# Kernel optimization log

Measured on AMD Instinct MI355X. Metric: run time of the kernel, lower is better.

The kernel has to match this reference:

```python
import jax, jax.numpy as jnp
import numpy as np

D_MODEL = 2048
N_HEADS = 16
D_HEAD = D_MODEL // N_HEADS
D_FF = 4 * D_MODEL
LN_EPS = 1e-5


def setup_inputs() -> dict:
    key = jax.random.key(0)
    ks = jax.random.split(key, 12)
    s = 1.0 / np.sqrt(D_MODEL)
    sf = 1.0 / np.sqrt(D_FF)
    return {
        "x": jax.random.normal(ks[0], (1, 2048, D_MODEL), dtype=jnp.float32),
        "ln1_g": jnp.ones((D_MODEL,), jnp.float32),
        "ln1_b": jnp.zeros((D_MODEL,), jnp.float32),
        # weights stored [in, out] (transpose of torch layout; equivalent under random init)
        "Wq": jax.random.normal(ks[1], (D_MODEL, D_MODEL), jnp.float32) * s,
        "Wk": jax.random.normal(ks[2], (D_MODEL, D_MODEL), jnp.float32) * s,
        "Wv": jax.random.normal(ks[3], (D_MODEL, D_MODEL), jnp.float32) * s,
        "Wp": jax.random.normal(ks[4], (D_MODEL, D_MODEL), jnp.float32) * s,
        "bp": jnp.zeros((D_MODEL,), jnp.float32),
        "ln2_g": jnp.ones((D_MODEL,), jnp.float32),
        "ln2_b": jnp.zeros((D_MODEL,), jnp.float32),
        "W1": jax.random.normal(ks[5], (D_MODEL, D_FF), jnp.float32) * s,
        "b1": jnp.zeros((D_FF,), jnp.float32),
        "W2": jax.random.normal(ks[6], (D_FF, D_MODEL), jnp.float32) * sf,
        "b2": jnp.zeros((D_MODEL,), jnp.float32),
    }


def _layer_norm(x, g, b):
    mu = jnp.mean(x, axis=-1, keepdims=True)
    var = jnp.mean(jnp.square(x - mu), axis=-1, keepdims=True)
    return (x - mu) * jax.lax.rsqrt(var + LN_EPS) * g + b


def _attention(h, Wq, Wk, Wv, Wp, bp):
    B, S, E = h.shape
    q = (h @ Wq).reshape(B, S, N_HEADS, D_HEAD)
    k = (h @ Wk).reshape(B, S, N_HEADS, D_HEAD)
    v = (h @ Wv).reshape(B, S, N_HEADS, D_HEAD)
    # [B, H, S, S] causal scores (matches the naive materialized original)
    scores = jnp.einsum("bqhd,bkhd->bhqk", q, k) / np.sqrt(D_HEAD).astype(np.float32)
    causal = jnp.arange(S)[:, None] >= jnp.arange(S)[None, :]
    scores = jnp.where(causal, scores, -jnp.inf)
    attn = jax.nn.softmax(scores, axis=-1)
    out = jnp.einsum("bhqk,bkhd->bqhd", attn, v).reshape(B, S, E)
    return out @ Wp + bp


def reference(x, ln1_g, ln1_b, Wq, Wk, Wv, Wp, bp, ln2_g, ln2_b, W1, b1, W2, b2):
    # attention branch: x += MHA(LN1(x)); dropout=0 (inference)
    x1 = x + _attention(_layer_norm(x, ln1_g, ln1_b), Wq, Wk, Wv, Wp, bp)
    # ff branch: FeedForward adds its own residual on the normalized input
    g = _layer_norm(x1, ln2_g, ln2_b)
    mlp = jax.nn.gelu(g @ W1 + b1, approximate=False) @ W2 + b2
    return x1 + (g + mlp)
```

## Files before the change

### kernel.cpp

```cpp
#include <hip/hip_runtime.h>
#include <math.h>

typedef unsigned int u32;
typedef unsigned short u16;
typedef __attribute__((ext_vector_type(8))) short short8;
typedef __attribute__((ext_vector_type(4))) float f32x4;

__device__ __forceinline__ u16 f2bf(float f) {
  u32 u = __builtin_bit_cast(u32, f);
  u += 0x7FFFu + ((u >> 16) & 1u);
  return (u16)(u >> 16);
}
__device__ __forceinline__ float bf2f(u16 h) {
  u32 u = ((u32)h) << 16;
  return __builtin_bit_cast(float, u);
}
__device__ __forceinline__ void gload_lds16(const void* g, void* l) {
  __builtin_amdgcn_global_load_lds((const __attribute__((address_space(1))) u32*)g,
                                   (__attribute__((address_space(3))) u32*)l, 16, 0, 0);
}
__device__ __forceinline__ f32x4 mfma16(short8 a, short8 b, f32x4 c) {
  return __builtin_amdgcn_mfma_f32_16x16x32_bf16(a, b, c, 0, 0, 0);
}

__global__ __launch_bounds__(256) void transpose_cast4(const float* __restrict__ Wq,
                                                       const float* __restrict__ Wk,
                                                       const float* __restrict__ Wv,
                                                       const float* __restrict__ Wp,
                                                       u16* __restrict__ wqkvT,
                                                       u16* __restrict__ wpT) {
  __shared__ __attribute__((aligned(16))) u16 tile[64][72];
  const int z = blockIdx.z;
  const float* src = (z == 0) ? Wq : (z == 1) ? Wk : (z == 2) ? Wv : Wp;
  u16* dst = (z < 3) ? (wqkvT + (size_t)z * 2048 * 2048) : wpT;
  const int n0 = blockIdx.x * 64, k0 = blockIdx.y * 64;
  const int t = threadIdx.x;
  const int tr = t >> 4;
  const int tc4 = (t & 15) * 4;
#pragma unroll
  for (int p = 0; p < 4; ++p) {
    int row = p * 16 + tr;
    const float4 v = *(const float4*)(src + (size_t)(k0 + row) * 2048 + n0 + tc4);
    tile[tc4 + 0][row] = f2bf(v.x);
    tile[tc4 + 1][row] = f2bf(v.y);
    tile[tc4 + 2][row] = f2bf(v.z);
    tile[tc4 + 3][row] = f2bf(v.w);
  }
  __syncthreads();
  const int nr = t >> 2;
  const int kc = (t & 3) * 16;
  u16* d = dst + (size_t)(n0 + nr) * 2048 + k0 + kc;
  *(short8*)(d) = *(const short8*)&tile[nr][kc];
  *(short8*)(d + 8) = *(const short8*)&tile[nr][kc + 8];
}

__global__ __launch_bounds__(256) void transpose_cast(const float* __restrict__ src,
                                                      u16* __restrict__ dst, int K, int N) {
  __shared__ __attribute__((aligned(16))) u16 tile[64][72];
  const int n0 = blockIdx.x * 64, k0 = blockIdx.y * 64;
  const int t = threadIdx.x;
  const int tr = t >> 4;
  const int tc4 = (t & 15) * 4;
#pragma unroll
  for (int p = 0; p < 4; ++p) {
    int row = p * 16 + tr;
    const float4 v = *(const float4*)(src + (size_t)(k0 + row) * N + n0 + tc4);
    tile[tc4 + 0][row] = f2bf(v.x);
    tile[tc4 + 1][row] = f2bf(v.y);
    tile[tc4 + 2][row] = f2bf(v.z);
    tile[tc4 + 3][row] = f2bf(v.w);
  }
  __syncthreads();
  const int nr = t >> 2;
  const int kc = (t & 3) * 16;
  u16* d = dst + (size_t)(n0 + nr) * K + k0 + kc;
  *(short8*)(d) = *(const short8*)&tile[nr][kc];
  *(short8*)(d + 8) = *(const short8*)&tile[nr][kc + 8];
}

__global__ __launch_bounds__(256) void transpose_v(const u16* __restrict__ qkv,
                                                   u16* __restrict__ vT) {
  __shared__ __attribute__((aligned(16))) u16 tile[64][72];
  const int kv0 = blockIdx.x * 64, d0 = blockIdx.y * 64, h = blockIdx.z;
  const int t = threadIdx.x;
  const int tr = t >> 3;
  const int tc8 = (t & 7) * 8;
#pragma unroll
  for (int p = 0; p < 2; ++p) {
    int row = p * 32 + tr;
    short8 v = *(const short8*)(qkv + (size_t)(kv0 + row) * 6144 + 4096 + h * 128 + d0 + tc8);
#pragma unroll
    for (int j = 0; j < 8; ++j) tile[tc8 + j][row] = (u16)v[j];
  }
  __syncthreads();
  const int dr = t >> 2;
  const int kc = (t & 3) * 16;
  u16* dst = vT + ((size_t)h * 128 + d0 + dr) * 2048 + kv0 + kc;
  *(short8*)dst = *(const short8*)&tile[dr][kc];
  *(short8*)(dst + 8) = *(const short8*)&tile[dr][kc + 8];
}

__global__ __launch_bounds__(256) void ln_kernel(const float* __restrict__ x,
                                                 const float* __restrict__ gw,
                                                 const float* __restrict__ bw,
                                                 u16* __restrict__ out) {
  const int row = blockIdx.x, t = threadIdx.x;
  const float* xr = x + (size_t)row * 2048;
  const float4 v0 = *(const float4*)(xr + t * 8);
  const float4 v1 = *(const float4*)(xr + t * 8 + 4);
  float s = v0.x + v0.y + v0.z + v0.w + v1.x + v1.y + v1.z + v1.w;
  float q = v0.x * v0.x + v0.y * v0.y + v0.z * v0.z + v0.w * v0.w +
            v1.x * v1.x + v1.y * v1.y + v1.z * v1.z + v1.w * v1.w;
#pragma unroll
  for (int w = 32; w; w >>= 1) { s += __shfl_xor(s, w); q += __shfl_xor(q, w); }
  __shared__ float rs[4], rq[4];
  const int wid = t >> 6, lane = t & 63;
  if (!lane) { rs[wid] = s; rq[wid] = q; }
  __syncthreads();
  s = rs[0] + rs[1] + rs[2] + rs[3];
  q = rq[0] + rq[1] + rq[2] + rq[3];
  const float mu = s * (1.f / 2048.f);
  const float var = q * (1.f / 2048.f) - mu * mu;
  const float rstd = rsqrtf(var + 1e-5f);
  const float4 g0 = *(const float4*)(gw + t * 8);
  const float4 g1 = *(const float4*)(gw + t * 8 + 4);
  const float4 b0 = *(const float4*)(bw + t * 8);
  const float4 b1 = *(const float4*)(bw + t * 8 + 4);
  short8 o;
  o[0] = (short)f2bf((v0.x - mu) * rstd * g0.x + b0.x);
  o[1] = (short)f2bf((v0.y - mu) * rstd * g0.y + b0.y);
  o[2] = (short)f2bf((v0.z - mu) * rstd * g0.z + b0.z);
  o[3] = (short)f2bf((v0.w - mu) * rstd * g0.w + b0.w);
  o[4] = (short)f2bf((v1.x - mu) * rstd * g1.x + b1.x);
  o[5] = (short)f2bf((v1.y - mu) * rstd * g1.y + b1.y);
  o[6] = (short)f2bf((v1.z - mu) * rstd * g1.z + b1.z);
  o[7] = (short)f2bf((v1.w - mu) * rstd * g1.w + b1.w);
  *(short8*)(out + (size_t)row * 2048 + t * 8) = o;
}

__global__ __launch_bounds__(256) void reduce_ln(const float* __restrict__ pA,
                                                 const float* __restrict__ pB,
                                                 const float* __restrict__ bias,
                                                 const float* __restrict__ res1,
                                                 const float* __restrict__ gw,
                                                 const float* __restrict__ bw,
                                                 float* __restrict__ x1,
                                                 u16* __restrict__ g) {
  const int row = blockIdx.x, t = threadIdx.x;
  const size_t MN = 4194304;
  const size_t base = (size_t)row * 2048 + t * 8;
  float v[8];
#pragma unroll
  for (int half = 0; half < 2; ++half) {
    float4 a0 = *(const float4*)(pA + base + half * 4);
    float4 a1 = *(const float4*)(pA + MN + base + half * 4);
    float4 b0 = *(const float4*)(pB + base + half * 4);
    float4 b1 = *(const float4*)(pB + MN + base + half * 4);
    float4 bi = *(const float4*)(bias + t * 8 + half * 4);
    float4 r1 = *(const float4*)(res1 + base + half * 4);
    v[half * 4 + 0] = a0.x + a1.x + b0.x + b1.x + bi.x + r1.x;
    v[half * 4 + 1] = a0.y + a1.y + b0.y + b1.y + bi.y + r1.y;
    v[half * 4 + 2] = a0.z + a1.z + b0.z + b1.z + bi.z + r1.z;
    v[half * 4 + 3] = a0.w + a1.w + b0.w + b1.w + bi.w + r1.w;
  }
  float4 o0 = {v[0], v[1], v[2], v[3]}, o1 = {v[4], v[5], v[6], v[7]};
  *(float4*)(x1 + base) = o0;
  *(float4*)(x1 + base + 4) = o1;
  float s = 0.f, q = 0.f;
#pragma unroll
  for (int j = 0; j < 8; ++j) { s += v[j]; q += v[j] * v[j]; }
#pragma unroll
  for (int w = 32; w; w >>= 1) { s += __shfl_xor(s, w); q += __shfl_xor(q, w); }
  __shared__ float rs[4], rq[4];
  const int wid = t >> 6, lane = t & 63;
  if (!lane) { rs[wid] = s; rq[wid] = q; }
  __syncthreads();
  s = rs[0] + rs[1] + rs[2] + rs[3];
  q = rq[0] + rq[1] + rq[2] + rq[3];
  const float mu = s * (1.f / 2048.f);
  const float var = q * (1.f / 2048.f) - mu * mu;
  const float rstd = rsqrtf(var + 1e-5f);
  short8 o;
#pragma unroll
  for (int j = 0; j < 8; ++j) {
    float gj = *(gw + t * 8 + j);
    float bj = *(bw + t * 8 + j);
    o[j] = (short)f2bf((v[j] - mu) * rstd * gj + bj);
  }
  *(short8*)(g + base) = o;
}

template <int EPI>
__global__ __launch_bounds__(512, 2) void gemm3(const u16* __restrict__ A,
                                                const u16* __restrict__ Bt,
                                                int M, int N, int K, int Kc,
                                                u16* __restrict__ outB,
                                                const float* __restrict__ bias,
                                                float* __restrict__ pA,
                                                float* __restrict__ pB) {
  __shared__ __attribute__((aligned(16))) u16 lds[3 * 16384];
  const int m0 = blockIdx.y * 256, n0 = blockIdx.x * 256;
  const int tid = threadIdx.x, wid = tid >> 6, lane = tid & 63;
  const int wr = wid >> 2, wc = wid & 3;
  const int lq = lane & 15, lk = lane >> 4;
  const int kStart = blockIdx.z * Kc;
  const int NT = Kc / 32;

  size_t aoff[2], boff[2];
#pragma unroll
  for (int s = 0; s < 2; ++s) {
    int c = s * 512 + tid;
    int row = c >> 2;
    int col = ((c & 3) ^ ((row >> 1) & 3)) * 8;
    aoff[s] = (size_t)(m0 + row) * K + kStart + col;
    boff[s] = (size_t)(n0 + row) * K + kStart + col;
  }
  u16* ldst = lds + tid * 8;

#define STA(s, buf, t2) gload_lds16(A + aoff[s] + (size_t)((t2) * 32), \
                                    ldst + (buf) * 16384 + (s) * 4096)
#define STB(s, buf, t2) gload_lds16(Bt + boff[s] + (size_t)((t2) * 32), \
                                    ldst + (buf) * 16384 + 8192 + (s) * 4096)

  STA(0, 0, 0); STA(1, 0, 0); STB(0, 0, 0); STB(1, 0, 0);
  STA(0, 1, 1); STA(1, 1, 1); STB(0, 1, 1); STB(1, 1, 1);
  asm volatile("s_waitcnt vmcnt(4)" ::: "memory");
  __builtin_amdgcn_s_barrier();
  __builtin_amdgcn_sched_barrier(0);

  f32x4 acc[8][4] = {};
  int cur = 0, nxt2 = 2;
  for (int t = 0; t < NT; ++t) {
    const char* bufc = (const char*)lds + cur * 32768;
    const bool st = (t + 2) < NT;
    short8 bf[4], af[4];
#pragma unroll
    for (int ni = 0; ni < 4; ++ni) {
      int br = wc * 64 + ni * 16 + lq;
      bf[ni] = *(const short8*)(bufc + 16384 + br * 64 + ((lk ^ ((br >> 1) & 3)) << 4));
    }
#pragma unroll
    for (int mi = 0; mi < 4; ++mi) {
      int ar = wr * 128 + mi * 16 + lq;
      af[mi] = *(const short8*)(bufc + ar * 64 + ((lk ^ ((ar >> 1) & 3)) << 4));
    }
    if (st) { STA(0, nxt2, t + 2); STA(1, nxt2, t + 2); }
    __builtin_amdgcn_s_setprio(1);
#pragma unroll
    for (int mi = 0; mi < 4; ++mi)
#pragma unroll
      for (int ni = 0; ni < 4; ++ni)
        acc[mi][ni] = mfma16(af[mi], bf[ni], acc[mi][ni]);
    __builtin_amdgcn_s_setprio(0);
#pragma unroll
    for (int mi = 0; mi < 4; ++mi) {
      int ar = wr * 128 + (mi + 4) * 16 + lq;
      af[mi] = *(const short8*)(bufc + ar * 64 + ((lk ^ ((ar >> 1) & 3)) << 4));
    }
    if (st) { STB(0, nxt2, t + 2); STB(1, nxt2, t + 2); }
    __builtin_amdgcn_s_setprio(1);
#pragma unroll
    for (int mi = 0; mi < 4; ++mi)
#pragma unroll
      for (int ni = 0; ni < 4; ++ni)
        acc[mi + 4][ni] = mfma16(af[mi], bf[ni], acc[mi + 4][ni]);
    __builtin_amdgcn_s_setprio(0);
    if (st) asm volatile("s_waitcnt vmcnt(4)" ::: "memory");
    else    asm volatile("s_waitcnt vmcnt(0)" ::: "memory");
    __builtin_amdgcn_s_barrier();
    __builtin_amdgcn_sched_barrier(0);
    cur = (cur == 2) ? 0 : cur + 1;
    nxt2 = (nxt2 == 2) ? 0 : nxt2 + 1;
  }
#undef STA
#undef STB

  float* pp = nullptr;
  if (EPI == 4) {
    pp = (blockIdx.z < 2 ? pA : pB) + (size_t)(blockIdx.z & 1) * ((size_t)M * N);
  }
#pragma unroll
  for (int mi = 0; mi < 8; ++mi) {
#pragma unroll
    for (int ni = 0; ni < 4; ++ni) {
      const int col = n0 + wc * 64 + ni * 16 + lq;
#pragma unroll
      for (int r = 0; r < 4; ++r) {
        const int row = m0 + wr * 128 + mi * 16 + lk * 4 + r;
        const size_t idx = (size_t)row * N + col;
        float v = acc[mi][ni][r];
        if (EPI == 0) {
          outB[idx] = f2bf(v);
        } else if (EPI == 2) {
          float xg = v + bias[col];
          outB[idx] = f2bf(0.5f * xg * (1.f + erff(xg * 0.70710678118654752f)));
        } else {
          pp[idx] = v;
        }
      }
    }
  }
}

template <int NS, int RES2>
__global__ __launch_bounds__(256) void reduce_kernel(const float* __restrict__ pA,
                                                     const float* __restrict__ pB,
                                                     const float* __restrict__ bias,
                                                     const float* __restrict__ res1,
                                                     const u16* __restrict__ res2,
                                                     float* __restrict__ out,
                                                     int MN, int N) {
  const int i = (blockIdx.x * 256 + threadIdx.x) * 4;
  if (i >= MN) return;
  float4 s = *(const float4*)(pA + i);
  {
    const float4 t = *(const float4*)(pA + MN + i);
    s.x += t.x; s.y += t.y; s.z += t.z; s.w += t.w;
  }
  if (NS == 4) {
    const float4 t0 = *(const float4*)(pB + i);
    const float4 t1 = *(const float4*)(pB + MN + i);
    s.x += t0.x + t1.x; s.y += t0.y + t1.y; s.z += t0.z + t1.z; s.w += t0.w + t1.w;
  }
  const int col = i & (N - 1);
  const float4 bv = *(const float4*)(bias + col);
  const float4 r1 = *(const float4*)(res1 + i);
  float4 o;
  o.x = s.x + bv.x + r1.x;
  o.y = s.y + bv.y + r1.y;
  o.z = s.z + bv.z + r1.z;
  o.w = s.w + bv.w + r1.w;
  if (RES2) {
    const u16* r2 = res2 + i;
    o.x += bf2f(r2[0]); o.y += bf2f(r2[1]); o.z += bf2f(r2[2]); o.w += bf2f(r2[3]);
  }
  *(float4*)(out + i) = o;
}

__global__ __launch_bounds__(256) void attn_kernel(const u16* __restrict__ qkv,
                                                   const u16* __restrict__ vT,
                                                   u16* __restrict__ attnout) {
  __shared__ __attribute__((aligned(16))) u16 lsK[2 * 64 * 128];
  __shared__ __attribute__((aligned(16))) u16 lsV[2 * 128 * 64];
  __shared__ __attribute__((aligned(16))) u16 lsP[4][16 * 64];
  const int h = blockIdx.x;
  const int qi = 31 - blockIdx.y;
  const int qb = qi * 64;
  const int tid = threadIdx.x, wid = tid >> 6, lane = tid & 63;
  const int lq = lane & 15, lk = lane >> 4;
  const int qw = qb + wid * 16;

  short8 qf[4];
  {
    const u16* qp = qkv + (size_t)(qw + lq) * 6144 + h * 128;
#pragma unroll
    for (int ks = 0; ks < 4; ++ks) qf[ks] = *(const short8*)(qp + ks * 32 + lk * 8);
  }
  float mreg[4], lreg[4];
  f32x4 o[8];
#pragma unroll
  for (int r = 0; r < 4; ++r) { mreg[r] = -INFINITY; lreg[r] = 0.f; }
#pragma unroll
  for (int dt = 0; dt < 8; ++dt) o[dt] = (f32x4){0.f, 0.f, 0.f, 0.f};

  const int rK = lane >> 4, sK = lane & 15;
  const int rV = lane >> 3, sV = lane & 7;
  const int nkt = qi + 1;

  auto STAGE = [&](int kt_, int b_) {
    const int kv0_ = kt_ * 64;
#pragma unroll
    for (int i = 0; i < 4; ++i) {
      int c = wid * 4 + i;
      int rowK = c * 4 + rK;
      gload_lds16(qkv + (size_t)(kv0_ + rowK) * 6144 + 2048 + h * 128 + ((sK ^ (rowK & 7)) * 8),
                  lsK + b_ * 8192 + c * 512);
      int rowV = c * 8 + rV;
      gload_lds16(vT + ((size_t)h * 128 + rowV) * 2048 + kv0_ + ((sV ^ (rowV & 7)) * 8),
                  lsV + b_ * 8192 + c * 512);
    }
  };

  STAGE(0, 0);
  for (int kt = 0; kt < nkt; ++kt) {
    const int b = kt & 1;
    const int kv0 = kt * 64;
    if (kt + 1 < nkt) {
      STAGE(kt + 1, b ^ 1);
      asm volatile("s_waitcnt vmcnt(8)" ::: "memory");
    } else {
      asm volatile("s_waitcnt vmcnt(0)" ::: "memory");
    }
    __builtin_amdgcn_s_barrier();
    __builtin_amdgcn_sched_barrier(0);
    const char* Kb = (const char*)(lsK + b * 8192);
    const char* Vb = (const char*)(lsV + b * 8192);

    f32x4 sc[4];
#pragma unroll
    for (int nt = 0; nt < 4; ++nt) sc[nt] = (f32x4){0.f, 0.f, 0.f, 0.f};
#pragma unroll
    for (int ks = 0; ks < 4; ++ks) {
#pragma unroll
      for (int nt = 0; nt < 4; ++nt) {
        int kvr = nt * 16 + lq;
        short8 kf = *(const short8*)(Kb + kvr * 256 +
                                     ((ks * 64 + lk * 16) ^ ((kvr & 7) << 4)));
        sc[nt] = mfma16(qf[ks], kf, sc[nt]);
      }
    }
    float rmax[4] = {-INFINITY, -INFINITY, -INFINITY, -INFINITY};
#pragma unroll
    for (int nt = 0; nt < 4; ++nt) {
      int kv = kv0 + nt * 16 + lq;
#pragma unroll
      for (int r = 0; r < 4; ++r) {
        int qrow = qw + lk * 4 + r;
        float s = (kv <= qrow) ? sc[nt][r] * 0.08838834764831845f : -INFINITY;
        sc[nt][r] = s;
        rmax[r] = fmaxf(rmax[r], s);
      }
    }
#pragma unroll
    for (int r = 0; r < 4; ++r)
#pragma unroll
      for (int w = 1; w < 16; w <<= 1) rmax[r] = fmaxf(rmax[r], __shfl_xor(rmax[r], w));
    bool grow = false;
#pragma unroll
    for (int r = 0; r < 4; ++r) grow |= (rmax[r] > mreg[r] + 8.f);
    if (__any(grow)) {
#pragma unroll
      for (int r = 0; r < 4; ++r) {
        float mn = fmaxf(mreg[r], rmax[r]);
        float alpha = __expf(mreg[r] - mn);
        mreg[r] = mn;
        lreg[r] *= alpha;
#pragma unroll
        for (int dt = 0; dt < 8; ++dt) o[dt][r] *= alpha;
      }
    }
    float rsum[4] = {0.f, 0.f, 0.f, 0.f};
    u16* P = &lsP[wid][0];
#pragma unroll
    for (int nt = 0; nt < 4; ++nt) {
#pragma unroll
      for (int r = 0; r < 4; ++r) {
        float p = __expf(sc[nt][r] - mreg[r]);
        rsum[r] += p;
        int prow = lk * 4 + r, pcol = nt * 16 + lq;
        *(u16*)((char*)P + prow * 128 + ((pcol * 2) ^ ((prow & 7) << 4))) = f2bf(p);
      }
    }
#pragma unroll
    for (int r = 0; r < 4; ++r) {
#pragma unroll
      for (int w = 1; w < 16; w <<= 1) rsum[r] += __shfl_xor(rsum[r], w);
      lreg[r] += rsum[r];
    }
#pragma unroll
    for (int kk = 0; kk < 2; ++kk) {
      short8 pa = *(const short8*)((const char*)P + lq * 128 +
                                   ((kk * 64 + lk * 16) ^ ((lq & 7) << 4)));
#pragma unroll
      for (int dt = 0; dt < 8; ++dt) {
        int dr = dt * 16 + lq;
        short8 vf = *(const short8*)(Vb + dr * 128 +
                                     ((kk * 64 + lk * 16) ^ ((dr & 7) << 4)));
        o[dt] = mfma16(pa, vf, o[dt]);
      }
    }
    __builtin_amdgcn_s_barrier();
  }
#pragma unroll
  for (int r = 0; r < 4; ++r) {
    float inv = 1.f / lreg[r];
    int row = qw + lk * 4 + r;
    u16* op = attnout + (size_t)row * 2048 + h * 128 + lq;
#pragma unroll
    for (int dt = 0; dt < 8; ++dt) op[dt * 16] = f2bf(o[dt][r] * inv);
  }
}

extern "C" void kernel_launch(void* const* d_in, const int* in_sizes, int n_in,
                              void* d_out, int out_size, void* d_ws, size_t ws_size,
                              hipStream_t stream) {
  (void)in_sizes; (void)n_in; (void)out_size; (void)ws_size;
  const float* x    = (const float*)d_in[0];
  const float* ln1g = (const float*)d_in[1];
  const float* ln1b = (const float*)d_in[2];
  const float* Wq   = (const float*)d_in[3];
  const float* Wk   = (const float*)d_in[4];
  const float* Wv   = (const float*)d_in[5];
  const float* Wp   = (const float*)d_in[6];
  const float* bp   = (const float*)d_in[7];
  const float* ln2g = (const float*)d_in[8];
  const float* ln2b = (const float*)d_in[9];
  const float* W1   = (const float*)d_in[10];
  const float* b1   = (const float*)d_in[11];
  const float* W2   = (const float*)d_in[12];
  const float* b2   = (const float*)d_in[13];
  float* out = (float*)d_out;
  char* ws = (char*)d_ws;

  u16* wqkvT = (u16*)(ws + 0);
  u16* hbuf  = (u16*)(ws + 25165824);
  u16* wpT   = (u16*)(ws + 33554432);
  u16* w1T   = (u16*)(ws + 41943040);
  u16* w2T   = (u16*)(ws + 75497472);
  u16* qkv   = (u16*)(ws + 109051904);
  u16* vT    = (u16*)(ws + 134217728);
  u16* attn  = (u16*)(ws + 142606336);
  float* x1  = (float*)(ws + 150994944);
  u16* g     = (u16*)(ws + 167772160);
  u16* ff1   = (u16*)(ws + 0);
  float* projPA = (float*)(ws + 0);
  float* projPB = (float*)(ws + 109051904);
  float* ffPA = (float*)(ws + 33554432);
  float* ffPB = (float*)(ws + 109051904);

  dim3 b256(256), b512(512);
  transpose_cast4<<<dim3(32, 32, 4), b256, 0, stream>>>(Wq, Wk, Wv, Wp, wqkvT, wpT);
  transpose_cast<<<dim3(128, 32), b256, 0, stream>>>(W1, w1T, 2048, 8192);
  transpose_cast<<<dim3(32, 128), b256, 0, stream>>>(W2, w2T, 8192, 2048);
  ln_kernel<<<2048, b256, 0, stream>>>(x, ln1g, ln1b, hbuf);
  gemm3<0><<<dim3(24, 8, 1), b512, 0, stream>>>(hbuf, wqkvT, 2048, 6144, 2048, 2048,
                                                qkv, nullptr, nullptr, nullptr);
  transpose_v<<<dim3(32, 2, 16), b256, 0, stream>>>(qkv, vT);
  attn_kernel<<<dim3(16, 32), b256, 0, stream>>>(qkv, vT, attn);
  gemm3<4><<<dim3(8, 8, 4), b512, 0, stream>>>(attn, wpT, 2048, 2048, 2048, 512,
                                               nullptr, nullptr, projPA, projPB);
  reduce_ln<<<2048, b256, 0, stream>>>(projPA, projPB, bp, x, ln2g, ln2b, x1, g);
  gemm3<2><<<dim3(32, 8, 1), b512, 0, stream>>>(g, w1T, 2048, 8192, 2048, 2048,
                                                ff1, b1, nullptr, nullptr);
  gemm3<4><<<dim3(8, 8, 4), b512, 0, stream>>>(ff1, w2T, 2048, 2048, 8192, 2048,
                                               nullptr, nullptr, ffPA, ffPB);
  reduce_kernel<4, 1><<<4096, b256, 0, stream>>>(ffPA, ffPB, b2, x1, g, out,
                                                 4194304, 2048);
}
```

Baseline: 413.2 us.

## Split attention KV range across two blocks with merge kernel; add smaller-tile QKV GEMM

Attention now splits each query tile's causal KV range into two chunks processed by separate blocks. Each block writes unnormalized fp32 partial outputs plus row max and sum, and a new merge kernel combines the two halves into bf16. The aim is more parallelism and better load balance for the causal workload. In exchange it drops the double-buffered K/V prefetch, and the extra fp32 partial traffic plus an added launch cost memory bandwidth. Separately, the QKV projection switches to a new gemm5 with 256x128 tiles and a 3-stage LDS pipeline, doubling the grid to raise occupancy.

```diff
diff --git a/kernel.cpp b/kernel.cpp
--- a/kernel.cpp
+++ b/kernel.cpp
@@ -302,6 +302,109 @@
   }
 }
 
+template <int EPI>
+__global__ __launch_bounds__(512, 4) void gemm5(const u16* __restrict__ A,
+                                                const u16* __restrict__ Bt,
+                                                int M, int N, int K, int Kc,
+                                                u16* __restrict__ outB,
+                                                const float* __restrict__ bias,
+                                                float* __restrict__ pA,
+                                                float* __restrict__ pB) {
+  __shared__ __attribute__((aligned(16))) u16 lds[3 * 12288];
+  const int m0 = blockIdx.y * 256, n0 = blockIdx.x * 128;
+  const int tid = threadIdx.x, wid = tid >> 6, lane = tid & 63;
+  const int wr = wid >> 1, wc = wid & 1;
+  const int lq = lane & 15, lk = lane >> 4;
+  const int kStart = blockIdx.z * Kc;
+  const int NT = Kc / 32;
+
+  size_t aoff[2], boff;
+#pragma unroll
+  for (int s = 0; s < 2; ++s) {
+    int c = s * 512 + tid;
+    int row = c >> 2;
+    int col = ((c & 3) ^ ((row >> 1) & 3)) * 8;
+    aoff[s] = (size_t)(m0 + row) * K + kStart + col;
+  }
+  {
+    int row = tid >> 2;
+    int col = ((tid & 3) ^ ((row >> 1) & 3)) * 8;
+    boff = (size_t)(n0 + row) * K + kStart + col;
+  }
+  u16* ldst = lds + tid * 8;
+
+#define STA(s, buf, t2) gload_lds16(A + aoff[s] + (size_t)((t2) * 32), \
+                                    ldst + (buf) * 12288 + (s) * 4096)
+#define STB(buf, t2) gload_lds16(Bt + boff + (size_t)((t2) * 32), \
+                                 ldst + (buf) * 12288 + 8192)
+
+  STA(0, 0, 0); STA(1, 0, 0); STB(0, 0);
+  STA(0, 1, 1); STA(1, 1, 1); STB(1, 1);
+  asm volatile("s_waitcnt vmcnt(3)" ::: "memory");
+  __builtin_amdgcn_s_barrier();
+  __builtin_amdgcn_sched_barrier(0);
+
+  f32x4 acc[4][4] = {};
+  int cur = 0, nxt2 = 2;
+  for (int t = 0; t < NT; ++t) {
+    const char* bufc = (const char*)lds + cur * 24576;
+    const bool st = (t + 2) < NT;
+    short8 bf[4], af[4];
+#pragma unroll
+    for (int ni = 0; ni < 4; ++ni) {
+      int br = wc * 64 + ni * 16 + lq;
+      bf[ni] = *(const short8*)(bufc + 16384 + br * 64 + ((lk ^ ((br >> 1) & 3)) << 4));
+    }
+#pragma unroll
+    for (int mi = 0; mi < 4; ++mi) {
+      int ar = wr * 64 + mi * 16 + lq;
+      af[mi] = *(const short8*)(bufc + ar * 64 + ((lk ^ ((ar >> 1) & 3)) << 4));
+    }
+    if (st) { STA(0, nxt2, t + 2); STA(1, nxt2, t + 2); STB(nxt2, t + 2); }
+    __builtin_amdgcn_s_setprio(1);
+#pragma unroll
+    for (int mi = 0; mi < 4; ++mi)
+#pragma unroll
+      for (int ni = 0; ni < 4; ++ni)
+        acc[mi][ni] = mfma16(af[mi], bf[ni], acc[mi][ni]);
+    __builtin_amdgcn_s_setprio(0);
+    if (st) asm volatile("s_waitcnt vmcnt(3)" ::: "memory");
+    else    asm volatile("s_waitcnt vmcnt(0)" ::: "memory");
+    __builtin_amdgcn_s_barrier();
+    __builtin_amdgcn_sched_barrier(0);
+    cur = (cur == 2) ? 0 : cur + 1;
+    nxt2 = (nxt2 == 2) ? 0 : nxt2 + 1;
+  }
+#undef STA
+#undef STB
+
+  float* pp = nullptr;
+  if (EPI == 4) {
+    pp = (blockIdx.z < 2 ? pA : pB) + (size_t)(blockIdx.z & 1) * ((size_t)M * N);
+  }
+#pragma unroll
+  for (int mi = 0; mi < 4; ++mi) {
+#pragma unroll
+    for (int ni = 0; ni < 4; ++ni) {
+      const int col = n0 + wc * 64 + ni * 16 + lq;
+#pragma unroll
+      for (int r = 0; r < 4; ++r) {
+        const int row = m0 + wr * 64 + mi * 16 + lk * 4 + r;
+        const size_t idx = (size_t)row * N + col;
+        float v = acc[mi][ni][r];
+        if (EPI == 0) {
+          outB[idx] = f2bf(v);
+        } else if (EPI == 2) {
+          float xg = v + bias[col];
+          outB[idx] = f2bf(0.5f * xg * (1.f + erff(xg * 0.70710678118654752f)));
+        } else {
+          pp[idx] = v;
+        }
+      }
+    }
+  }
+}
+
 template <int NS, int RES2>
 __global__ __launch_bounds__(256) void reduce_kernel(const float* __restrict__ pA,
                                                      const float* __restrict__ pB,
@@ -339,17 +442,25 @@
 
 __global__ __launch_bounds__(256) void attn_kernel(const u16* __restrict__ qkv,
                                                    const u16* __restrict__ vT,
-                                                   u16* __restrict__ attnout) {
-  __shared__ __attribute__((aligned(16))) u16 lsK[2 * 64 * 128];
-  __shared__ __attribute__((aligned(16))) u16 lsV[2 * 128 * 64];
+                                                   float* __restrict__ po,
+                                                   float* __restrict__ pm,
+                                                   float* __restrict__ pl) {
+  __shared__ __attribute__((aligned(16))) u16 lsK[64 * 128];
+  __shared__ __attribute__((aligned(16))) u16 lsV[128 * 64];
   __shared__ __attribute__((aligned(16))) u16 lsP[4][16 * 64];
   const int h = blockIdx.x;
-  const int qi = 31 - blockIdx.y;
+  const int c = blockIdx.y;
+  const int qi = 31 - blockIdx.z;
   const int qb = qi * 64;
   const int tid = threadIdx.x, wid = tid >> 6, lane = tid & 63;
   const int lq = lane & 15, lk = lane >> 4;
   const int qw = qb + wid * 16;
 
+  const int nkt = qi + 1;
+  const int ch0 = (nkt + 1) >> 1;
+  const int base = c ? ch0 : 0;
+  const int cnt = c ? (nkt - ch0) : ch0;
+
   short8 qf[4];
   {
     const u16* qp = qkv + (size_t)(qw + lq) * 6144 + h * 128;
@@ -365,36 +476,21 @@
 
   const int rK = lane >> 4, sK = lane & 15;
   const int rV = lane >> 3, sV = lane & 7;
-  const int nkt = qi + 1;
-
-  auto STAGE = [&](int kt_, int b_) {
-    const int kv0_ = kt_ * 64;
+  for (int it = 0; it < cnt; ++it) {
+    const int kt = base + it;
+    const int kv0 = kt * 64;
+    if (it) __syncthreads();
 #pragma unroll
     for (int i = 0; i < 4; ++i) {
-      int c = wid * 4 + i;
-      int rowK = c * 4 + rK;
-      gload_lds16(qkv + (size_t)(kv0_ + rowK) * 6144 + 2048 + h * 128 + ((sK ^ (rowK & 7)) * 8),
-                  lsK + b_ * 8192 + c * 512);
-      int rowV = c * 8 + rV;
-      gload_lds16(vT + ((size_t)h * 128 + rowV) * 2048 + kv0_ + ((sV ^ (rowV & 7)) * 8),
-                  lsV + b_ * 8192 + c * 512);
-    }
-  };
-
-  STAGE(0, 0);
-  for (int kt = 0; kt < nkt; ++kt) {
-    const int b = kt & 1;
-    const int kv0 = kt * 64;
-    if (kt + 1 < nkt) {
-      STAGE(kt + 1, b ^ 1);
-      asm volatile("s_waitcnt vmcnt(8)" ::: "memory");
-    } else {
-      asm volatile("s_waitcnt vmcnt(0)" ::: "memory");
-    }
-    __builtin_amdgcn_s_barrier();
-    __builtin_amdgcn_sched_barrier(0);
-    const char* Kb = (const char*)(lsK + b * 8192);
-    const char* Vb = (const char*)(lsV + b * 8192);
+      int cc = wid * 4 + i;
+      int rowK = cc * 4 + rK;
+      gload_lds16(qkv + (size_t)(kv0 + rowK) * 6144 + 2048 + h * 128 + ((sK ^ (rowK & 7)) * 8),
+                  lsK + cc * 512);
+      int rowV = cc * 8 + rV;
+      gload_lds16(vT + ((size_t)h * 128 + rowV) * 2048 + kv0 + ((sV ^ (rowV & 7)) * 8),
+                  lsV + cc * 512);
+    }
+    __syncthreads();
 
     f32x4 sc[4];
 #pragma unroll
@@ -404,7 +500,7 @@
 #pragma unroll
       for (int nt = 0; nt < 4; ++nt) {
         int kvr = nt * 16 + lq;
-        short8 kf = *(const short8*)(Kb + kvr * 256 +
+        short8 kf = *(const short8*)((const char*)lsK + kvr * 256 +
                                      ((ks * 64 + lk * 16) ^ ((kvr & 7) << 4)));
         sc[nt] = mfma16(qf[ks], kf, sc[nt]);
       }
@@ -464,21 +560,45 @@
 #pragma unroll
       for (int dt = 0; dt < 8; ++dt) {
         int dr = dt * 16 + lq;
-        short8 vf = *(const short8*)(Vb + dr * 128 +
+        short8 vf = *(const short8*)((const char*)lsV + dr * 128 +
                                      ((kk * 64 + lk * 16) ^ ((dr & 7) << 4)));
         o[dt] = mfma16(pa, vf, o[dt]);
       }
     }
-    __builtin_amdgcn_s_barrier();
   }
 #pragma unroll
   for (int r = 0; r < 4; ++r) {
-    float inv = 1.f / lreg[r];
     int row = qw + lk * 4 + r;
-    u16* op = attnout + (size_t)row * 2048 + h * 128 + lq;
-#pragma unroll
-    for (int dt = 0; dt < 8; ++dt) op[dt * 16] = f2bf(o[dt][r] * inv);
-  }
+    float* op = po + (size_t)c * 4194304 + ((size_t)h * 2048 + row) * 128 + lq;
+#pragma unroll
+    for (int dt = 0; dt < 8; ++dt) op[dt * 16] = o[dt][r];
+    if (lq == 0) {
+      pm[c * 32768 + h * 2048 + row] = mreg[r];
+      pl[c * 32768 + h * 2048 + row] = lreg[r];
+    }
+  }
+}
+
+__global__ __launch_bounds__(256) void attn_merge(const float* __restrict__ po,
+                                                  const float* __restrict__ pm,
+                                                  const float* __restrict__ pl,
+                                                  u16* __restrict__ attn) {
+  const int e = (blockIdx.x * 256 + threadIdx.x) * 4;
+  const int hrow = e >> 7;
+  const int d = e & 127;
+  const int h = hrow >> 11, row = hrow & 2047;
+  float m0 = pm[hrow], m1 = pm[32768 + hrow];
+  float l0 = pl[hrow], l1 = pl[32768 + hrow];
+  float m = fmaxf(m0, m1);
+  float w0 = __expf(m0 - m), w1 = __expf(m1 - m);
+  float inv = 1.f / (l0 * w0 + l1 * w1);
+  float4 o0 = *(const float4*)(po + e);
+  float4 o1 = *(const float4*)(po + 4194304 + e);
+  u16* op = attn + (size_t)row * 2048 + h * 128 + d;
+  op[0] = f2bf((o0.x * w0 + o1.x * w1) * inv);
+  op[1] = f2bf((o0.y * w0 + o1.y * w1) * inv);
+  op[2] = f2bf((o0.z * w0 + o1.z * w1) * inv);
+  op[3] = f2bf((o0.w * w0 + o1.w * w1) * inv);
 }
 
 extern "C" void kernel_launch(void* const* d_in, const int* in_sizes, int n_in,
@@ -513,6 +633,9 @@
   float* x1  = (float*)(ws + 150994944);
   u16* g     = (u16*)(ws + 167772160);
   u16* ff1   = (u16*)(ws + 0);
+  float* po = (float*)(ws + 0);
+  float* pm = (float*)(ws + 167772160);
+  float* pl = (float*)(ws + 167772160 + 262144);
   float* projPA = (float*)(ws + 0);
   float* projPB = (float*)(ws + 109051904);
   float* ffPA = (float*)(ws + 33554432);
@@ -523,10 +646,11 @@
   transpose_cast<<<dim3(128, 32), b256, 0, stream>>>(W1, w1T, 2048, 8192);
   transpose_cast<<<dim3(32, 128), b256, 0, stream>>>(W2, w2T, 8192, 2048);
   ln_kernel<<<2048, b256, 0, stream>>>(x, ln1g, ln1b, hbuf);
-  gemm3<0><<<dim3(24, 8, 1), b512, 0, stream>>>(hbuf, wqkvT, 2048, 6144, 2048, 2048,
+  gemm5<0><<<dim3(48, 8, 1), b512, 0, stream>>>(hbuf, wqkvT, 2048, 6144, 2048, 2048,
                                                 qkv, nullptr, nullptr, nullptr);
   transpose_v<<<dim3(32, 2, 16), b256, 0, stream>>>(qkv, vT);
-  attn_kernel<<<dim3(16, 32), b256, 0, stream>>>(qkv, vT, attn);
+  attn_kernel<<<dim3(16, 2, 32), b256, 0, stream>>>(qkv, vT, po, pm, pl);
+  attn_merge<<<4096, b256, 0, stream>>>(po, pm, pl, attn);
   gemm3<4><<<dim3(8, 8, 4), b512, 0, stream>>>(attn, wpT, 2048, 2048, 2048, 512,
                                                nullptr, nullptr, projPA, projPB);
   reduce_ln<<<2048, b256, 0, stream>>>(projPA, projPB, bp, x, ln2g, ln2b, x1, g);
```

Measured after the change: 404.5 us. 2.1% less time.
